# Optimization experiments

Hardware: AMD Instinct MI355X
Metric: run time of the kernel (lower is better)

The kernel has to match this reference:

```python
import jax, jax.numpy as jnp
import numpy as np

N = 100000
E = 1600000
IN_DIM, HID_DIM, OUT_DIM = 128, 128, 64


def setup_inputs() -> dict:
    key = jax.random.key(0)
    ks = jax.random.split(key, 8)
    x = jax.random.normal(ks[0], (N, IN_DIM), dtype=jnp.float32)
    edge_index = jax.random.randint(ks[1], (2, E), 0, N, dtype=jnp.int64)
    s = 1.0 / np.sqrt(IN_DIM)
    W1 = jax.random.normal(ks[2], (IN_DIM, HID_DIM), dtype=jnp.float32) * s
    Wd1 = jax.random.normal(ks[3], (IN_DIM, HID_DIM), dtype=jnp.float32) * s
    s2 = 1.0 / np.sqrt(HID_DIM)
    W2 = jax.random.normal(ks[4], (HID_DIM, OUT_DIM), dtype=jnp.float32) * s2
    Wd2 = jax.random.normal(ks[5], (HID_DIM, OUT_DIM), dtype=jnp.float32) * s2
    alpha1 = jnp.full((1,), 0.5, dtype=jnp.float32)
    beta1 = jnp.full((1,), 0.5, dtype=jnp.float32)
    alpha2 = jnp.full((1,), 0.5, dtype=jnp.float32)
    beta2 = jnp.full((1,), 0.5, dtype=jnp.float32)
    return dict(x=x, edge_index=edge_index, W1=W1, Wd1=Wd1, alpha1=alpha1,
                beta1=beta1, W2=W2, Wd2=Wd2, alpha2=alpha2, beta2=beta2)


def _edge_weights(row, col, num_nodes, dtype):
    # D_out^{-1/2} A D_in^{-1/2} expressed per-edge
    ones = jnp.ones(row.shape[0], dtype=dtype)
    deg_out = jax.ops.segment_sum(ones, row, num_segments=num_nodes)
    deg_in = jax.ops.segment_sum(ones, col, num_segments=num_nodes)
    inv_sqrt = lambda d: jnp.where(d > 0, jax.lax.rsqrt(jnp.maximum(d, 1.0)), 0.0)
    return inv_sqrt(deg_out)[row] * inv_sqrt(deg_in)[col]


def _dir_conv(x, row, col, edge_w, num_nodes, W, Wd, alpha, beta):
    transformed = x @ W                       # [N, out]
    msg = transformed[col] * edge_w[:, None]  # gather + scale, [E, out]
    h_base = jax.ops.segment_sum(msg, row, num_segments=num_nodes)
    h_dir = alpha * transformed + beta * (x @ Wd)
    return h_base + h_dir


def reference(x, edge_index, W1, Wd1, alpha1, beta1, W2, Wd2, alpha2, beta2):
    row, col = edge_index[0], edge_index[1]
    num_nodes = x.shape[0]
    edge_w = _edge_weights(row, col, num_nodes, x.dtype)
    h = _dir_conv(x, row, col, edge_w, num_nodes, W1, Wd1, alpha1, beta1)
    h = jax.nn.relu(h)
    # dropout is identity in eval mode
    out = _dir_conv(h, row, col, edge_w, num_nodes, W2, Wd2, alpha2, beta2)
    return out
```

## Files before the change

### kernel.cpp

```cpp
#include <hip/hip_runtime.h>

#define N_NODES 100000
#define N_EDGES 1600000
#define ELL_W   64

typedef __attribute__((ext_vector_type(8))) short bf16x8;
typedef __attribute__((ext_vector_type(4))) float f32x4;

__device__ __forceinline__ unsigned short rne16(float x) {
    unsigned u = __float_as_uint(x);
    u += 0x7fffu + ((u >> 16) & 1u);
    return (unsigned short)(u >> 16);
}
__device__ __forceinline__ float bf16_lo(unsigned u) { return __uint_as_float(u << 16); }
__device__ __forceinline__ float bf16_hi(unsigned u) { return __uint_as_float(u & 0xffff0000u); }

__device__ __forceinline__ void wprep_elem(const float* __restrict__ W, int Mcols, int idx,
                                           unsigned short* __restrict__ Wh,
                                           unsigned short* __restrict__ Wl) {
    int m = idx % Mcols, k = idx / Mcols;
    float w = W[idx];
    unsigned short h = rne16(w);
    float hf = __uint_as_float((unsigned)h << 16);
    Wh[m * 128 + k] = h;
    Wl[m * 128 + k] = rne16(w - hf);
}

__global__ __launch_bounds__(256) void prep_kernel(const float* __restrict__ W1,
                                                   const float* __restrict__ Wd1,
                                                   const float* __restrict__ W2,
                                                   const float* __restrict__ Wd2,
                                                   unsigned short* __restrict__ w1h, unsigned short* __restrict__ w1l,
                                                   unsigned short* __restrict__ wd1h, unsigned short* __restrict__ wd1l,
                                                   unsigned short* __restrict__ w2h, unsigned short* __restrict__ w2l,
                                                   unsigned short* __restrict__ wd2h, unsigned short* __restrict__ wd2l,
                                                   unsigned* __restrict__ cnt) {
    int i = blockIdx.x * 256 + threadIdx.x;
    if (i < 16384)            wprep_elem(W1, 128, i, w1h, w1l);
    else if (i < 32768)       wprep_elem(Wd1, 128, i - 16384, wd1h, wd1l);
    else if (i < 40960)       wprep_elem(W2, 64, i - 32768, w2h, w2l);
    else if (i < 49152)       wprep_elem(Wd2, 64, i - 40960, wd2h, wd2l);
    else if (i < 49152 + 2 * N_NODES) cnt[i - 49152] = 0u;
}

__global__ __launch_bounds__(256) void build_ell4(const int* __restrict__ ei,
                                                  unsigned* __restrict__ cnt_out,
                                                  unsigned* __restrict__ cnt_in,
                                                  int* __restrict__ ell) {
    int t = blockIdx.x * 256 + threadIdx.x;
    int e0 = t * 4;
    if (e0 >= N_EDGES) return;
    int4 r4 = *(const int4*)&ei[e0];
    int4 c4 = *(const int4*)&ei[N_EDGES + e0];
    unsigned p0 = atomicAdd(&cnt_out[r4.x], 1u);
    unsigned p1 = atomicAdd(&cnt_out[r4.y], 1u);
    unsigned p2 = atomicAdd(&cnt_out[r4.z], 1u);
    unsigned p3 = atomicAdd(&cnt_out[r4.w], 1u);
    atomicAdd(&cnt_in[c4.x], 1u);
    atomicAdd(&cnt_in[c4.y], 1u);
    atomicAdd(&cnt_in[c4.z], 1u);
    atomicAdd(&cnt_in[c4.w], 1u);
    if (p0 < ELL_W) ell[(size_t)r4.x * ELL_W + p0] = c4.x;
    if (p1 < ELL_W) ell[(size_t)r4.y * ELL_W + p1] = c4.y;
    if (p2 < ELL_W) ell[(size_t)r4.z * ELL_W + p2] = c4.z;
    if (p3 < ELL_W) ell[(size_t)r4.w * ELL_W + p3] = c4.w;
}

__global__ __launch_bounds__(256) void dinv_kernel(const unsigned* __restrict__ deg_out,
                                                   const unsigned* __restrict__ deg_in,
                                                   float* __restrict__ dinv_out,
                                                   float* __restrict__ dinv_in) {
    int n = blockIdx.x * 256 + threadIdx.x;
    if (n >= N_NODES) return;
    unsigned d0 = deg_out[n];
    unsigned d1 = deg_in[n];
    dinv_out[n] = d0 ? rsqrtf((float)d0) : 0.0f;
    dinv_in[n]  = d1 ? rsqrtf((float)d1) : 0.0f;
}

template <int M, bool SCALE_T>
__device__ __forceinline__ void gemm_body(const float* __restrict__ A,
                                          const unsigned short* __restrict__ Wah,
                                          const unsigned short* __restrict__ Wal,
                                          const unsigned short* __restrict__ Wbh,
                                          const unsigned short* __restrict__ Wbl,
                                          const float* __restrict__ alpha,
                                          const float* __restrict__ beta,
                                          const float* __restrict__ dinv_in,
                                          unsigned short* __restrict__ Tb,
                                          float* __restrict__ Hd,
                                          int bid) {
    constexpr int NI = M / 64;
    __shared__ unsigned short sH[64 * 128];
    __shared__ unsigned short sL[64 * 128];

    const int tid = threadIdx.x;
    const int w = tid >> 6;
    const int lane = tid & 63;
    const int rowBase = bid * 64;

    #pragma unroll
    for (int it = 0; it < 8; ++it) {
        int flat = it * 256 + tid;
        int r = flat >> 5, c4 = flat & 31;
        int gr = rowBase + r;
        float4 v = make_float4(0.f, 0.f, 0.f, 0.f);
        if (gr < N_NODES) v = *(const float4*)&A[(size_t)gr * 128 + c4 * 4];
        unsigned short hx = rne16(v.x), hy = rne16(v.y), hz = rne16(v.z), hw = rne16(v.w);
        float lx = v.x - __uint_as_float((unsigned)hx << 16);
        float ly = v.y - __uint_as_float((unsigned)hy << 16);
        float lz = v.z - __uint_as_float((unsigned)hz << 16);
        float lw = v.w - __uint_as_float((unsigned)hw << 16);
        uint2 hi2, lo2;
        hi2.x = (unsigned)hx | ((unsigned)hy << 16);
        hi2.y = (unsigned)hz | ((unsigned)hw << 16);
        lo2.x = (unsigned)rne16(lx) | ((unsigned)rne16(ly) << 16);
        lo2.y = (unsigned)rne16(lz) | ((unsigned)rne16(lw) << 16);
        unsigned byte = (unsigned)(r * 256 + c4 * 8) ^ ((unsigned)(r & 7) << 4);
        *(uint2*)((char*)sH + byte) = hi2;
        *(uint2*)((char*)sL + byte) = lo2;
    }
    __syncthreads();

    const int colBase = w * (16 * NI);
    const int g  = lane >> 4;
    const int ln = lane & 15;
    const unsigned swz = ((unsigned)(ln & 7)) << 4;

    f32x4 acc[2][4][NI] = {};

    #pragma unroll
    for (int ks = 0; ks < 4; ++ks) {
        bf16x8 ah[4], al[4];
        #pragma unroll
        for (int mi = 0; mi < 4; ++mi) {
            unsigned byte = ((unsigned)((mi * 16 + ln) * 256 + ks * 64 + g * 16)) ^ swz;
            ah[mi] = *(const bf16x8*)((const char*)sH + byte);
            al[mi] = *(const bf16x8*)((const char*)sL + byte);
        }
        #pragma unroll
        for (int mat = 0; mat < 2; ++mat) {
            const unsigned short* __restrict__ Wh = mat ? Wbh : Wah;
            const unsigned short* __restrict__ Wl = mat ? Wbl : Wal;
            #pragma unroll
            for (int ni = 0; ni < NI; ++ni) {
                int col = colBase + ni * 16 + ln;
                size_t off = (size_t)col * 128 + ks * 32 + g * 8;
                bf16x8 wh = *(const bf16x8*)&Wh[off];
                bf16x8 wl = *(const bf16x8*)&Wl[off];
                #pragma unroll
                for (int mi = 0; mi < 4; ++mi) {
                    acc[mat][mi][ni] = __builtin_amdgcn_mfma_f32_16x16x32_bf16(ah[mi], wh, acc[mat][mi][ni], 0, 0, 0);
                    acc[mat][mi][ni] = __builtin_amdgcn_mfma_f32_16x16x32_bf16(al[mi], wh, acc[mat][mi][ni], 0, 0, 0);
                    acc[mat][mi][ni] = __builtin_amdgcn_mfma_f32_16x16x32_bf16(ah[mi], wl, acc[mat][mi][ni], 0, 0, 0);
                }
            }
        }
    }

    const float al_ = alpha[0], be_ = beta[0];
    #pragma unroll
    for (int mi = 0; mi < 4; ++mi) {
        #pragma unroll
        for (int ni = 0; ni < NI; ++ni) {
            #pragma unroll
            for (int r = 0; r < 4; ++r) {
                int row = rowBase + mi * 16 + g * 4 + r;
                if (row >= N_NODES) continue;
                int col = colBase + ni * 16 + ln;
                float t = acc[0][mi][ni][r];
                float d = fmaf(al_, t, be_ * acc[1][mi][ni][r]);
                float ts = SCALE_T ? dinv_in[row] * t : t;
                Tb[(size_t)row * M + col] = rne16(ts);
                Hd[(size_t)row * M + col] = d;
            }
        }
    }
}

__global__ __launch_bounds__(256) void gemm1_kernel(const float* __restrict__ A,
                                                    const unsigned short* __restrict__ Wah,
                                                    const unsigned short* __restrict__ Wal,
                                                    const unsigned short* __restrict__ Wbh,
                                                    const unsigned short* __restrict__ Wbl,
                                                    const float* __restrict__ alpha,
                                                    const float* __restrict__ beta,
                                                    unsigned short* __restrict__ Tb,
                                                    float* __restrict__ Hd) {
    gemm_body<128, false>(A, Wah, Wal, Wbh, Wbl, alpha, beta, nullptr, Tb, Hd, blockIdx.x);
}

__global__ __launch_bounds__(256) void gemm2_kernel(const float* __restrict__ A,
                                                    const unsigned short* __restrict__ Wah,
                                                    const unsigned short* __restrict__ Wal,
                                                    const unsigned short* __restrict__ Wbh,
                                                    const unsigned short* __restrict__ Wbl,
                                                    const float* __restrict__ alpha,
                                                    const float* __restrict__ beta,
                                                    const float* __restrict__ dinv_in,
                                                    unsigned short* __restrict__ Tb,
                                                    float* __restrict__ Hd) {
    gemm_body<64, true>(A, Wah, Wal, Wbh, Wbl, alpha, beta, dinv_in, Tb, Hd, blockIdx.x);
}

__global__ __launch_bounds__(256) void agg_kernel_128(const unsigned* __restrict__ deg,
                                                      const int* __restrict__ ell,
                                                      const float* __restrict__ dinv_out,
                                                      const float* __restrict__ dinv_in,
                                                      const unsigned* __restrict__ Tb,
                                                      float* __restrict__ H) {
    int node = blockIdx.x * 4 + (threadIdx.x >> 6);
    if (node >= N_NODES) return;
    int lane = threadIdx.x & 63;
    unsigned d = deg[node];
    if (d > ELL_W) d = ELL_W;
    const int* __restrict__ cl = &ell[(size_t)node * ELL_W];
    float dn = dinv_out[node];
    float2* __restrict__ Hv = (float2*)H;
    float2 acc = Hv[(size_t)node * 64 + lane];
    unsigned i = 0;
    for (; i + 4 <= d; i += 4) {
        int c0 = cl[i], c1 = cl[i + 1], c2 = cl[i + 2], c3 = cl[i + 3];
        float w0 = dn * dinv_in[c0];
        float w1 = dn * dinv_in[c1];
        float w2 = dn * dinv_in[c2];
        float w3 = dn * dinv_in[c3];
        unsigned u0 = Tb[(size_t)c0 * 64 + lane];
        unsigned u1 = Tb[(size_t)c1 * 64 + lane];
        unsigned u2 = Tb[(size_t)c2 * 64 + lane];
        unsigned u3 = Tb[(size_t)c3 * 64 + lane];
        acc.x = fmaf(w0, bf16_lo(u0), acc.x); acc.y = fmaf(w0, bf16_hi(u0), acc.y);
        acc.x = fmaf(w1, bf16_lo(u1), acc.x); acc.y = fmaf(w1, bf16_hi(u1), acc.y);
        acc.x = fmaf(w2, bf16_lo(u2), acc.x); acc.y = fmaf(w2, bf16_hi(u2), acc.y);
        acc.x = fmaf(w3, bf16_lo(u3), acc.x); acc.y = fmaf(w3, bf16_hi(u3), acc.y);
    }
    for (; i < d; ++i) {
        int c0 = cl[i];
        float w0 = dn * dinv_in[c0];
        unsigned u0 = Tb[(size_t)c0 * 64 + lane];
        acc.x = fmaf(w0, bf16_lo(u0), acc.x); acc.y = fmaf(w0, bf16_hi(u0), acc.y);
    }
    acc.x = fmaxf(acc.x, 0.0f);
    acc.y = fmaxf(acc.y, 0.0f);
    Hv[(size_t)node * 64 + lane] = acc;
}

__global__ __launch_bounds__(256) void agg_kernel_64(const unsigned* __restrict__ deg,
                                                     const int* __restrict__ ell,
                                                     const float* __restrict__ dinv_out,
                                                     const unsigned short* __restrict__ Tb,
                                                     float* __restrict__ Out) {
    int node = blockIdx.x * 4 + (threadIdx.x >> 6);
    if (node >= N_NODES) return;
    int lane = threadIdx.x & 63;
    unsigned d = deg[node];
    if (d > ELL_W) d = ELL_W;
    const int* __restrict__ cl = &ell[(size_t)node * ELL_W];
    float dn = dinv_out[node];
    float acc = 0.0f;
    unsigned i = 0;
    for (; i + 4 <= d; i += 4) {
        int c0 = cl[i], c1 = cl[i + 1], c2 = cl[i + 2], c3 = cl[i + 3];
        float t0 = __uint_as_float(((unsigned)Tb[(size_t)c0 * 64 + lane]) << 16);
        float t1 = __uint_as_float(((unsigned)Tb[(size_t)c1 * 64 + lane]) << 16);
        float t2 = __uint_as_float(((unsigned)Tb[(size_t)c2 * 64 + lane]) << 16);
        float t3 = __uint_as_float(((unsigned)Tb[(size_t)c3 * 64 + lane]) << 16);
        acc += t0 + t1;
        acc += t2 + t3;
    }
    for (; i < d; ++i) {
        acc += __uint_as_float(((unsigned)Tb[(size_t)cl[i] * 64 + lane]) << 16);
    }
    Out[(size_t)node * 64 + lane] = fmaf(dn, acc, Out[(size_t)node * 64 + lane]);
}

extern "C" void kernel_launch(void* const* d_in, const int* in_sizes, int n_in,
                              void* d_out, int out_size, void* d_ws, size_t ws_size,
                              hipStream_t stream) {
    const float* x   = (const float*)d_in[0];
    const int*   ei  = (const int*)d_in[1];
    const float* W1  = (const float*)d_in[2];
    const float* Wd1 = (const float*)d_in[3];
    const float* a1  = (const float*)d_in[4];
    const float* b1  = (const float*)d_in[5];
    const float* W2  = (const float*)d_in[6];
    const float* Wd2 = (const float*)d_in[7];
    const float* a2  = (const float*)d_in[8];
    const float* b2  = (const float*)d_in[9];
    float* out = (float*)d_out;

    char* ws = (char*)d_ws;
    size_t off = 0;
    auto alloc = [&](size_t bytes) -> void* {
        void* p = ws + off;
        off = (off + bytes + 255) & ~(size_t)255;
        return p;
    };

    unsigned* cnt_out = (unsigned*)alloc(2 * sizeof(unsigned) * N_NODES);
    unsigned* cnt_in  = cnt_out + N_NODES;
    float* dinv_out   = (float*)alloc(sizeof(float) * N_NODES);
    float* dinv_in    = (float*)alloc(sizeof(float) * N_NODES);
    int* ell          = (int*)alloc(sizeof(int) * (size_t)N_NODES * ELL_W);
    unsigned* T1      = (unsigned*)alloc(sizeof(unsigned) * (size_t)N_NODES * 64);
    float* H1         = (float*)alloc(sizeof(float) * (size_t)N_NODES * 128);
    unsigned* T2      = (unsigned*)alloc(sizeof(unsigned) * (size_t)N_NODES * 32);
    unsigned short* wt1a_h = (unsigned short*)alloc(sizeof(short) * 128 * 128);
    unsigned short* wt1a_l = (unsigned short*)alloc(sizeof(short) * 128 * 128);
    unsigned short* wt1b_h = (unsigned short*)alloc(sizeof(short) * 128 * 128);
    unsigned short* wt1b_l = (unsigned short*)alloc(sizeof(short) * 128 * 128);
    unsigned short* wt2a_h = (unsigned short*)alloc(sizeof(short) * 64 * 128);
    unsigned short* wt2a_l = (unsigned short*)alloc(sizeof(short) * 64 * 128);
    unsigned short* wt2b_h = (unsigned short*)alloc(sizeof(short) * 64 * 128);
    unsigned short* wt2b_l = (unsigned short*)alloc(sizeof(short) * 64 * 128);

    const int prep_total = 49152 + 2 * N_NODES;
    prep_kernel<<<(prep_total + 255) / 256, 256, 0, stream>>>(
        W1, Wd1, W2, Wd2, wt1a_h, wt1a_l, wt1b_h, wt1b_l,
        wt2a_h, wt2a_l, wt2b_h, wt2b_l, cnt_out);

    const int gblocks = (N_NODES + 63) / 64;

    const int bblocks = (N_EDGES / 4 + 255) / 256;
    build_ell4<<<bblocks, 256, 0, stream>>>(ei, cnt_out, cnt_in, ell);

    gemm1_kernel<<<gblocks, 256, 0, stream>>>(x, wt1a_h, wt1a_l, wt1b_h, wt1b_l,
                                              a1, b1, (unsigned short*)T1, H1);

    dinv_kernel<<<(N_NODES + 255) / 256, 256, 0, stream>>>(cnt_out, cnt_in, dinv_out, dinv_in);

    agg_kernel_128<<<(N_NODES + 3) / 4, 256, 0, stream>>>(cnt_out, ell, dinv_out, dinv_in, T1, H1);

    gemm2_kernel<<<gblocks, 256, 0, stream>>>(H1, wt2a_h, wt2a_l, wt2b_h, wt2b_l, a2, b2,
                                              dinv_in, (unsigned short*)T2, out);
    agg_kernel_64<<<(N_NODES + 3) / 4, 256, 0, stream>>>(cnt_out, ell, dinv_out,
                                                         (const unsigned short*)T2, out);
}
```

Measured before the change: 385.5 us.

## Store hidden layer in bf16, fold degree scaling into GEMMs, drop dinv kernel

The hidden activation H1 is now stored as bf16 instead of fp32, so gemm2 loads a bf16 A tile and skips the low-part split and its extra MFMA pass. Layer-1 T is pre-scaled by the in-degree factor inside gemm1, which removes the per-edge dinv_in gather in the first aggregation. The separate dinv kernel is removed and rsqrt is computed inline from the counts. This cuts memory traffic and MFMA work, at the cost of bf16 rounding error on the hidden layer.

```diff
diff --git a/kernel.cpp b/kernel.cpp
--- a/kernel.cpp
+++ b/kernel.cpp
@@ -11,6 +11,9 @@
     unsigned u = __float_as_uint(x);
     u += 0x7fffu + ((u >> 16) & 1u);
     return (unsigned short)(u >> 16);
+}
+__device__ __forceinline__ unsigned pack_bf16x2(float a, float b) {
+    return (unsigned)rne16(a) | ((unsigned)rne16(b) << 16);
 }
 __device__ __forceinline__ float bf16_lo(unsigned u) { return __uint_as_float(u << 16); }
 __device__ __forceinline__ float bf16_hi(unsigned u) { return __uint_as_float(u & 0xffff0000u); }
@@ -66,59 +69,62 @@
     if (p3 < ELL_W) ell[(size_t)r4.w * ELL_W + p3] = c4.w;
 }
 
-__global__ __launch_bounds__(256) void dinv_kernel(const unsigned* __restrict__ deg_out,
-                                                   const unsigned* __restrict__ deg_in,
-                                                   float* __restrict__ dinv_out,
-                                                   float* __restrict__ dinv_in) {
-    int n = blockIdx.x * 256 + threadIdx.x;
-    if (n >= N_NODES) return;
-    unsigned d0 = deg_out[n];
-    unsigned d1 = deg_in[n];
-    dinv_out[n] = d0 ? rsqrtf((float)d0) : 0.0f;
-    dinv_in[n]  = d1 ? rsqrtf((float)d1) : 0.0f;
-}
-
-template <int M, bool SCALE_T>
-__device__ __forceinline__ void gemm_body(const float* __restrict__ A,
+template <int M, bool A_BF16, bool HD_BF16>
+__device__ __forceinline__ void gemm_body(const void* __restrict__ Avoid,
                                           const unsigned short* __restrict__ Wah,
                                           const unsigned short* __restrict__ Wal,
                                           const unsigned short* __restrict__ Wbh,
                                           const unsigned short* __restrict__ Wbl,
                                           const float* __restrict__ alpha,
                                           const float* __restrict__ beta,
-                                          const float* __restrict__ dinv_in,
+                                          const unsigned* __restrict__ cnt_in,
                                           unsigned short* __restrict__ Tb,
-                                          float* __restrict__ Hd,
+                                          void* __restrict__ Hdvoid,
                                           int bid) {
     constexpr int NI = M / 64;
     __shared__ unsigned short sH[64 * 128];
-    __shared__ unsigned short sL[64 * 128];
+    __shared__ unsigned short sL[A_BF16 ? 1 : 64 * 128];
 
     const int tid = threadIdx.x;
     const int w = tid >> 6;
     const int lane = tid & 63;
     const int rowBase = bid * 64;
 
-    #pragma unroll
-    for (int it = 0; it < 8; ++it) {
-        int flat = it * 256 + tid;
-        int r = flat >> 5, c4 = flat & 31;
-        int gr = rowBase + r;
-        float4 v = make_float4(0.f, 0.f, 0.f, 0.f);
-        if (gr < N_NODES) v = *(const float4*)&A[(size_t)gr * 128 + c4 * 4];
-        unsigned short hx = rne16(v.x), hy = rne16(v.y), hz = rne16(v.z), hw = rne16(v.w);
-        float lx = v.x - __uint_as_float((unsigned)hx << 16);
-        float ly = v.y - __uint_as_float((unsigned)hy << 16);
-        float lz = v.z - __uint_as_float((unsigned)hz << 16);
-        float lw = v.w - __uint_as_float((unsigned)hw << 16);
-        uint2 hi2, lo2;
-        hi2.x = (unsigned)hx | ((unsigned)hy << 16);
-        hi2.y = (unsigned)hz | ((unsigned)hw << 16);
-        lo2.x = (unsigned)rne16(lx) | ((unsigned)rne16(ly) << 16);
-        lo2.y = (unsigned)rne16(lz) | ((unsigned)rne16(lw) << 16);
-        unsigned byte = (unsigned)(r * 256 + c4 * 8) ^ ((unsigned)(r & 7) << 4);
-        *(uint2*)((char*)sH + byte) = hi2;
-        *(uint2*)((char*)sL + byte) = lo2;
+    if constexpr (A_BF16) {
+        const unsigned short* __restrict__ A = (const unsigned short*)Avoid;
+        #pragma unroll
+        for (int it = 0; it < 4; ++it) {
+            int flat = it * 256 + tid;
+            int r = flat >> 4, c8 = flat & 15;
+            int gr = rowBase + r;
+            uint4 v = make_uint4(0u, 0u, 0u, 0u);
+            if (gr < N_NODES) v = *(const uint4*)&A[(size_t)gr * 128 + c8 * 8];
+            unsigned byte = (unsigned)(r * 256 + c8 * 16) ^ ((unsigned)(r & 7) << 4);
+            *(uint4*)((char*)sH + byte) = v;
+        }
+    } else {
+        const float* __restrict__ A = (const float*)Avoid;
+        #pragma unroll
+        for (int it = 0; it < 8; ++it) {
+            int flat = it * 256 + tid;
+            int r = flat >> 5, c4 = flat & 31;
+            int gr = rowBase + r;
+            float4 v = make_float4(0.f, 0.f, 0.f, 0.f);
+            if (gr < N_NODES) v = *(const float4*)&A[(size_t)gr * 128 + c4 * 4];
+            unsigned short hx = rne16(v.x), hy = rne16(v.y), hz = rne16(v.z), hw = rne16(v.w);
+            float lx = v.x - __uint_as_float((unsigned)hx << 16);
+            float ly = v.y - __uint_as_float((unsigned)hy << 16);
+            float lz = v.z - __uint_as_float((unsigned)hz << 16);
+            float lw = v.w - __uint_as_float((unsigned)hw << 16);
+            uint2 hi2, lo2;
+            hi2.x = (unsigned)hx | ((unsigned)hy << 16);
+            hi2.y = (unsigned)hz | ((unsigned)hw << 16);
+            lo2.x = (unsigned)rne16(lx) | ((unsigned)rne16(ly) << 16);
+            lo2.y = (unsigned)rne16(lz) | ((unsigned)rne16(lw) << 16);
+            unsigned byte = (unsigned)(r * 256 + c4 * 8) ^ ((unsigned)(r & 7) << 4);
+            *(uint2*)((char*)sH + byte) = hi2;
+            *(uint2*)((char*)sL + byte) = lo2;
+        }
     }
     __syncthreads();
 
@@ -136,7 +142,7 @@
         for (int mi = 0; mi < 4; ++mi) {
             unsigned byte = ((unsigned)((mi * 16 + ln) * 256 + ks * 64 + g * 16)) ^ swz;
             ah[mi] = *(const bf16x8*)((const char*)sH + byte);
-            al[mi] = *(const bf16x8*)((const char*)sL + byte);
+            if constexpr (!A_BF16) al[mi] = *(const bf16x8*)((const char*)sL + byte);
         }
         #pragma unroll
         for (int mat = 0; mat < 2; ++mat) {
@@ -145,13 +151,14 @@
             #pragma unroll
             for (int ni = 0; ni < NI; ++ni) {
                 int col = colBase + ni * 16 + ln;
-                size_t off = (size_t)col * 128 + ks * 32 + g * 8;
-                bf16x8 wh = *(const bf16x8*)&Wh[off];
-                bf16x8 wl = *(const bf16x8*)&Wl[off];
+                size_t woff = (size_t)col * 128 + ks * 32 + g * 8;
+                bf16x8 wh = *(const bf16x8*)&Wh[woff];
+                bf16x8 wl = *(const bf16x8*)&Wl[woff];
                 #pragma unroll
                 for (int mi = 0; mi < 4; ++mi) {
                     acc[mat][mi][ni] = __builtin_amdgcn_mfma_f32_16x16x32_bf16(ah[mi], wh, acc[mat][mi][ni], 0, 0, 0);
-                    acc[mat][mi][ni] = __builtin_amdgcn_mfma_f32_16x16x32_bf16(al[mi], wh, acc[mat][mi][ni], 0, 0, 0);
+                    if constexpr (!A_BF16)
+                        acc[mat][mi][ni] = __builtin_amdgcn_mfma_f32_16x16x32_bf16(al[mi], wh, acc[mat][mi][ni], 0, 0, 0);
                     acc[mat][mi][ni] = __builtin_amdgcn_mfma_f32_16x16x32_bf16(ah[mi], wl, acc[mat][mi][ni], 0, 0, 0);
                 }
             }
@@ -162,17 +169,21 @@
     #pragma unroll
     for (int mi = 0; mi < 4; ++mi) {
         #pragma unroll
-        for (int ni = 0; ni < NI; ++ni) {
+        for (int r = 0; r < 4; ++r) {
+            int row = rowBase + mi * 16 + g * 4 + r;
+            if (row >= N_NODES) continue;
+            unsigned dIn = cnt_in[row];
+            float sc = dIn ? rsqrtf((float)dIn) : 0.0f;
             #pragma unroll
-            for (int r = 0; r < 4; ++r) {
-                int row = rowBase + mi * 16 + g * 4 + r;
-                if (row >= N_NODES) continue;
+            for (int ni = 0; ni < NI; ++ni) {
                 int col = colBase + ni * 16 + ln;
                 float t = acc[0][mi][ni][r];
                 float d = fmaf(al_, t, be_ * acc[1][mi][ni][r]);
-                float ts = SCALE_T ? dinv_in[row] * t : t;
-                Tb[(size_t)row * M + col] = rne16(ts);
-                Hd[(size_t)row * M + col] = d;
+                Tb[(size_t)row * M + col] = rne16(sc * t);
+                if constexpr (HD_BF16)
+                    ((unsigned short*)Hdvoid)[(size_t)row * M + col] = rne16(d);
+                else
+                    ((float*)Hdvoid)[(size_t)row * M + col] = d;
             }
         }
     }
@@ -185,78 +196,71 @@
                                                     const unsigned short* __restrict__ Wbl,
                                                     const float* __restrict__ alpha,
                                                     const float* __restrict__ beta,
+                                                    const unsigned* __restrict__ cnt_in,
                                                     unsigned short* __restrict__ Tb,
-                                                    float* __restrict__ Hd) {
-    gemm_body<128, false>(A, Wah, Wal, Wbh, Wbl, alpha, beta, nullptr, Tb, Hd, blockIdx.x);
-}
-
-__global__ __launch_bounds__(256) void gemm2_kernel(const float* __restrict__ A,
+                                                    unsigned short* __restrict__ H1) {
+    gemm_body<128, false, true>(A, Wah, Wal, Wbh, Wbl, alpha, beta, cnt_in, Tb, H1, blockIdx.x);
+}
+
+__global__ __launch_bounds__(256) void gemm2_kernel(const unsigned short* __restrict__ A,
                                                     const unsigned short* __restrict__ Wah,
                                                     const unsigned short* __restrict__ Wal,
                                                     const unsigned short* __restrict__ Wbh,
                                                     const unsigned short* __restrict__ Wbl,
                                                     const float* __restrict__ alpha,
                                                     const float* __restrict__ beta,
-                                                    const float* __restrict__ dinv_in,
+                                                    const unsigned* __restrict__ cnt_in,
                                                     unsigned short* __restrict__ Tb,
                                                     float* __restrict__ Hd) {
-    gemm_body<64, true>(A, Wah, Wal, Wbh, Wbl, alpha, beta, dinv_in, Tb, Hd, blockIdx.x);
-}
-
-__global__ __launch_bounds__(256) void agg_kernel_128(const unsigned* __restrict__ deg,
+    gemm_body<64, true, false>(A, Wah, Wal, Wbh, Wbl, alpha, beta, cnt_in, Tb, Hd, blockIdx.x);
+}
+
+__global__ __launch_bounds__(256) void agg_kernel_128(const unsigned* __restrict__ cnt_out,
                                                       const int* __restrict__ ell,
-                                                      const float* __restrict__ dinv_out,
-                                                      const float* __restrict__ dinv_in,
                                                       const unsigned* __restrict__ Tb,
-                                                      float* __restrict__ H) {
+                                                      unsigned* __restrict__ H1) {
     int node = blockIdx.x * 4 + (threadIdx.x >> 6);
     if (node >= N_NODES) return;
     int lane = threadIdx.x & 63;
-    unsigned d = deg[node];
-    if (d > ELL_W) d = ELL_W;
+    unsigned dfull = cnt_out[node];
+    float dn = dfull ? rsqrtf((float)dfull) : 0.0f;
+    unsigned d = dfull > ELL_W ? ELL_W : dfull;
     const int* __restrict__ cl = &ell[(size_t)node * ELL_W];
-    float dn = dinv_out[node];
-    float2* __restrict__ Hv = (float2*)H;
-    float2 acc = Hv[(size_t)node * 64 + lane];
+    float sx = 0.0f, sy = 0.0f;
     unsigned i = 0;
     for (; i + 4 <= d; i += 4) {
         int c0 = cl[i], c1 = cl[i + 1], c2 = cl[i + 2], c3 = cl[i + 3];
-        float w0 = dn * dinv_in[c0];
-        float w1 = dn * dinv_in[c1];
-        float w2 = dn * dinv_in[c2];
-        float w3 = dn * dinv_in[c3];
         unsigned u0 = Tb[(size_t)c0 * 64 + lane];
         unsigned u1 = Tb[(size_t)c1 * 64 + lane];
         unsigned u2 = Tb[(size_t)c2 * 64 + lane];
         unsigned u3 = Tb[(size_t)c3 * 64 + lane];
-        acc.x = fmaf(w0, bf16_lo(u0), acc.x); acc.y = fmaf(w0, bf16_hi(u0), acc.y);
-        acc.x = fmaf(w1, bf16_lo(u1), acc.x); acc.y = fmaf(w1, bf16_hi(u1), acc.y);
-        acc.x = fmaf(w2, bf16_lo(u2), acc.x); acc.y = fmaf(w2, bf16_hi(u2), acc.y);
-        acc.x = fmaf(w3, bf16_lo(u3), acc.x); acc.y = fmaf(w3, bf16_hi(u3), acc.y);
+        sx += bf16_lo(u0) + bf16_lo(u1);
+        sy += bf16_hi(u0) + bf16_hi(u1);
+        sx += bf16_lo(u2) + bf16_lo(u3);
+        sy += bf16_hi(u2) + bf16_hi(u3);
     }
     for (; i < d; ++i) {
-        int c0 = cl[i];
-        float w0 = dn * dinv_in[c0];
-        unsigned u0 = Tb[(size_t)c0 * 64 + lane];
-        acc.x = fmaf(w0, bf16_lo(u0), acc.x); acc.y = fmaf(w0, bf16_hi(u0), acc.y);
-    }
-    acc.x = fmaxf(acc.x, 0.0f);
-    acc.y = fmaxf(acc.y, 0.0f);
-    Hv[(size_t)node * 64 + lane] = acc;
-}
-
-__global__ __launch_bounds__(256) void agg_kernel_64(const unsigned* __restrict__ deg,
+        unsigned u0 = Tb[(size_t)cl[i] * 64 + lane];
+        sx += bf16_lo(u0);
+        sy += bf16_hi(u0);
+    }
+    unsigned hu = H1[(size_t)node * 64 + lane];
+    float fx = fmaxf(fmaf(dn, sx, bf16_lo(hu)), 0.0f);
+    float fy = fmaxf(fmaf(dn, sy, bf16_hi(hu)), 0.0f);
+    H1[(size_t)node * 64 + lane] = pack_bf16x2(fx, fy);
+}
+
+__global__ __launch_bounds__(256) void agg_kernel_64(const unsigned* __restrict__ cnt_out,
                                                      const int* __restrict__ ell,
-                                                     const float* __restrict__ dinv_out,
                                                      const unsigned short* __restrict__ Tb,
                                                      float* __restrict__ Out) {
     int node = blockIdx.x * 4 + (threadIdx.x >> 6);
     if (node >= N_NODES) return;
     int lane = threadIdx.x & 63;
-    unsigned d = deg[node];
-    if (d > ELL_W) d = ELL_W;
+    unsigned dfull = cnt_out[node];
+    float dn = dfull ? rsqrtf((float)dfull) : 0.0f;
+    unsigned d = dfull > ELL_W ? ELL_W : dfull;
     const int* __restrict__ cl = &ell[(size_t)node * ELL_W];
-    float dn = dinv_out[node];
     float acc = 0.0f;
     unsigned i = 0;
     for (; i + 4 <= d; i += 4) {
@@ -299,12 +303,10 @@
 
     unsigned* cnt_out = (unsigned*)alloc(2 * sizeof(unsigned) * N_NODES);
     unsigned* cnt_in  = cnt_out + N_NODES;
-    float* dinv_out   = (float*)alloc(sizeof(float) * N_NODES);
-    float* dinv_in    = (float*)alloc(sizeof(float) * N_NODES);
     int* ell          = (int*)alloc(sizeof(int) * (size_t)N_NODES * ELL_W);
-    unsigned* T1      = (unsigned*)alloc(sizeof(unsigned) * (size_t)N_NODES * 64);
-    float* H1         = (float*)alloc(sizeof(float) * (size_t)N_NODES * 128);
-    unsigned* T2      = (unsigned*)alloc(sizeof(unsigned) * (size_t)N_NODES * 32);
+    unsigned short* T1 = (unsigned short*)alloc(sizeof(short) * (size_t)N_NODES * 128);
+    unsigned short* H1 = (unsigned short*)alloc(sizeof(short) * (size_t)N_NODES * 128);
+    unsigned short* T2 = (unsigned short*)alloc(sizeof(short) * (size_t)N_NODES * 64);
     unsigned short* wt1a_h = (unsigned short*)alloc(sizeof(short) * 128 * 128);
     unsigned short* wt1a_l = (unsigned short*)alloc(sizeof(short) * 128 * 128);
     unsigned short* wt1b_h = (unsigned short*)alloc(sizeof(short) * 128 * 128);
@@ -319,20 +321,20 @@
         W1, Wd1, W2, Wd2, wt1a_h, wt1a_l, wt1b_h, wt1b_l,
         wt2a_h, wt2a_l, wt2b_h, wt2b_l, cnt_out);
 
-    const int gblocks = (N_NODES + 63) / 64;
-
     const int bblocks = (N_EDGES / 4 + 255) / 256;
     build_ell4<<<bblocks, 256, 0, stream>>>(ei, cnt_out, cnt_in, ell);
 
+    const int gblocks = (N_NODES + 63) / 64;
+
     gemm1_kernel<<<gblocks, 256, 0, stream>>>(x, wt1a_h, wt1a_l, wt1b_h, wt1b_l,
-                                              a1, b1, (unsigned short*)T1, H1);
-
-    dinv_kernel<<<(N_NODES + 255) / 256, 256, 0, stream>>>(cnt_out, cnt_in, dinv_out, dinv_in);
-
-    agg_kernel_128<<<(N_NODES + 3) / 4, 256, 0, stream>>>(cnt_out, ell, dinv_out, dinv_in, T1, H1);
-
-    gemm2_kernel<<<gblocks, 256, 0, stream>>>(H1, wt2a_h, wt2a_l, wt2b_h, wt2b_l, a2, b2,
-                                              dinv_in, (unsigned short*)T2, out);
-    agg_kernel_64<<<(N_NODES + 3) / 4, 256, 0, stream>>>(cnt_out, ell, dinv_out,
+                                              a1, b1, cnt_in, T1, H1);
+
+    agg_kernel_128<<<(N_NODES + 3) / 4, 256, 0, stream>>>(cnt_out, ell, (const unsigned*)T1,
+                                                          (unsigned*)H1);
+
+    gemm2_kernel<<<gblocks, 256, 0, stream>>>(H1, wt2a_h, wt2a_l, wt2b_h, wt2b_l,
+                                              a2, b2, cnt_in, T2, out);
+
+    agg_kernel_64<<<(N_NODES + 3) / 4, 256, 0, stream>>>(cnt_out, ell,
                                                          (const unsigned short*)T2, out);
 }
```

After: 374.2 us. 1.03x faster.
